# Optimization experiments

Hardware: AMD Instinct MI355X
Metric: run time of the kernel (lower is better)

## Reference

```python
import jax, jax.numpy as jnp
import numpy as np

B, N, F_IN, D, NBLOCKS = 16, 1024, 3, 128, 15
EPS = 1e-5


def setup_inputs() -> dict:
    key = jax.random.key(0)
    ks = jax.random.split(key, 8)
    inputs = jax.random.normal(ks[0], (B, N, F_IN), dtype=jnp.float32)
    # Row-normalized random adjacency as the graph operator L (spectral norm <= 1)
    A = jax.random.uniform(ks[1], (B, N, N), dtype=jnp.float32)
    L = A / jnp.sum(A, axis=-1, keepdims=True)
    mask = (jax.random.uniform(ks[2], (B, N, 1)) < 0.8).astype(jnp.float32)
    mask = mask.at[:, 0, :].set(1.0)  # ensure no empty graph
    W1 = jax.random.normal(ks[3], (F_IN, D), dtype=jnp.float32) / np.sqrt(F_IN)
    b1 = jnp.zeros((D,), jnp.float32)
    W_blocks = jax.random.normal(ks[4], (NBLOCKS, D, D), dtype=jnp.float32) / np.sqrt(D)
    b_blocks = jnp.zeros((NBLOCKS, D), jnp.float32)
    gamma_blocks = jnp.ones((NBLOCKS, D), jnp.float32)
    beta_blocks = jnp.zeros((NBLOCKS, D), jnp.float32)
    gamma1 = jnp.ones((D,), jnp.float32)
    beta1 = jnp.zeros((D,), jnp.float32)
    gamma2 = jnp.ones((D,), jnp.float32)
    beta2 = jnp.zeros((D,), jnp.float32)
    W2 = jax.random.normal(ks[5], (D, D), dtype=jnp.float32) / np.sqrt(D)
    b2 = jnp.zeros((D,), jnp.float32)
    return dict(inputs=inputs, L=L, mask=mask, W1=W1, b1=b1,
                W_blocks=W_blocks, b_blocks=b_blocks,
                gamma_blocks=gamma_blocks, beta_blocks=beta_blocks,
                gamma1=gamma1, beta1=beta1, gamma2=gamma2, beta2=beta2,
                W2=W2, b2=b2)


def _graph_bn(x, gamma, beta):
    # BatchNorm over (batch, nodes) per feature channel (training-mode stats)
    mean = jnp.mean(x, axis=(0, 1), keepdims=True)
    var = jnp.var(x, axis=(0, 1), keepdims=True)
    return (x - mean) * jax.lax.rsqrt(var + EPS) * gamma + beta


def reference(inputs, L, mask, W1, b1, W_blocks, b_blocks,
              gamma_blocks, beta_blocks, gamma1, beta1, gamma2, beta2,
              W2, b2):
    # conv1 (GraphConv k=1): per-node linear
    x1 = jnp.einsum('bnf,fd->bnd', inputs, W1) + b1          # [B,N,D]
    x2 = jnp.zeros_like(x1)

    def step(carry, params):
        a, b_prev = carry
        W, bias, g, be = params
        h = jax.nn.elu(_graph_bn(a, g, be))
        h = jnp.einsum('bnm,bmd->bnd', L, h)                 # Laplacian aggregation
        h = jnp.einsum('bnd,de->bne', h, W) + bias           # LapConv transform
        return (b_prev + h, a), None

    (x1, x2), _ = jax.lax.scan(step, (x1, x2),
                               (W_blocks, b_blocks, gamma_blocks, beta_blocks))

    x = jax.nn.elu(_graph_bn(x1, gamma1, beta1) + _graph_bn(x2, gamma2, beta2))
    # Dropout2d is identity in deterministic/eval reference
    x = jnp.einsum('bnd,de->bne', x, W2) + b2                # conv2 (k=1)
    # masked mean pool over nodes: mask [B,N,1] broadcasts over D
    out = jnp.sum(x * mask, axis=1) / jnp.sum(mask, axis=1)  # [B,D]
    return out
```

## Files before the change

### kernel.cpp

```cpp
#include <hip/hip_runtime.h>

typedef float f32x4 __attribute__((ext_vector_type(4)));
typedef __bf16 bf16x8 __attribute__((ext_vector_type(8)));
typedef unsigned int u32x4 __attribute__((ext_vector_type(4)));
typedef unsigned int u32x2 __attribute__((ext_vector_type(2)));
typedef unsigned short u16;

#define DEV __device__ __forceinline__

DEV u16 f2bf(float f) {
    unsigned int x = __float_as_uint(f);
    x += 0x7fffu + ((x >> 16) & 1u);
    return (u16)(x >> 16);
}
DEV unsigned pk2(float a, float b) {
    return (unsigned)f2bf(a) | ((unsigned)f2bf(b) << 16);
}
DEV float elu(float x) { return x > 0.f ? x : expm1f(x); }

DEV void gload16(const u16* g, void* l) {
    __builtin_amdgcn_global_load_lds(
        (const __attribute__((address_space(1))) unsigned int*)g,
        (__attribute__((address_space(3))) unsigned int*)l,
        16, 0, 0);
}

DEV float aload(const float* p) {
    return __hip_atomic_load(p, __ATOMIC_RELAXED, __HIP_MEMORY_SCOPE_AGENT);
}
DEV void astore(float* p, float v) {
    __hip_atomic_store(p, v, __ATOMIC_RELAXED, __HIP_MEMORY_SCOPE_AGENT);
}

DEV void barw(unsigned* ctr, unsigned cnt) {
    asm volatile("s_waitcnt vmcnt(0) lgkmcnt(0)" ::: "memory");
    __syncthreads();
    if (threadIdx.x == 0) {
        unsigned old = __hip_atomic_fetch_add(ctr, 1u, __ATOMIC_RELAXED,
                                              __HIP_MEMORY_SCOPE_AGENT);
        unsigned tgt = old - (old % cnt) + cnt;
        while (__hip_atomic_load(ctr, __ATOMIC_RELAXED,
                                 __HIP_MEMORY_SCOPE_AGENT) < tgt)
            __builtin_amdgcn_s_sleep(4);
    }
    __syncthreads();
}

constexpr float INV_M = 1.f / 16384.f;
constexpr float EPSV  = 1e-5f;

__global__ __launch_bounds__(256) void k_prep(
        const float* __restrict__ in, const float* __restrict__ L,
        const float* __restrict__ W1, const float* __restrict__ b1,
        const float* __restrict__ Wb,
        u16* __restrict__ Lb, u16* __restrict__ WT,
        float* __restrict__ xA, float* __restrict__ xB,
        float* __restrict__ SP0) {
    int t = threadIdx.x, bid = blockIdx.x;
    {
        long base = (long)bid * 1024;
#pragma unroll
        for (int j = 0; j < 4; ++j) {
            long i = (base + j * 256 + t) * 8;
            f32x4 a = *(const f32x4*)(L + i);
            f32x4 b = *(const f32x4*)(L + i + 4);
            u32x4 v;
            v[0] = pk2(a[0], a[1]); v[1] = pk2(a[2], a[3]);
            v[2] = pk2(b[0], b[1]); v[3] = pk2(b[2], b[3]);
            *(u32x4*)(Lb + i) = v;
        }
    }
    if (bid < 960) {
        int o = bid * 256 + t;
        int kk = o >> 14, r = o & 16383, e = r >> 7, d = r & 127;
        WT[o] = f2bf(Wb[(kk << 14) + (d << 7) + e]);
    }
    if (bid >= 1024 && bid < 1280) {
        __shared__ float red[2][8][128];
        int ib = bid - 1024;
        long R = (long)ib * 64;
        int c4 = (t & 31) * 4, rg = t >> 5;
        float w0[4], w1v[4], w2v[4], bb4[4];
#pragma unroll
        for (int c = 0; c < 4; ++c) {
            w0[c] = W1[c4 + c]; w1v[c] = W1[128 + c4 + c];
            w2v[c] = W1[256 + c4 + c]; bb4[c] = b1[c4 + c];
        }
        float s[4] = {}, q[4] = {};
#pragma unroll
        for (int i = 0; i < 8; ++i) {
            long grow = R + rg + 8 * i;
            float f0 = in[grow * 3], f1 = in[grow * 3 + 1], f2 = in[grow * 3 + 2];
            f32x4 v, z = {0.f, 0.f, 0.f, 0.f};
#pragma unroll
            for (int c = 0; c < 4; ++c) {
                float val = f0 * w0[c] + f1 * w1v[c] + f2 * w2v[c] + bb4[c];
                v[c] = val; s[c] += val; q[c] += val * val;
            }
            *(f32x4*)(xA + grow * 128 + c4) = v;
            *(f32x4*)(xB + grow * 128 + c4) = z;
        }
#pragma unroll
        for (int c = 0; c < 4; ++c) { red[0][rg][c4 + c] = s[c]; red[1][rg][c4 + c] = q[c]; }
        __syncthreads();
        if (t < 128) {
            float a = 0;
#pragma unroll
            for (int g = 0; g < 8; ++g) a += red[0][g][t];
            atomicAdd(&SP0[(ib & 15) * 256 + t], a);
        } else {
            int c = t - 128; float a = 0;
#pragma unroll
            for (int g = 0; g < 8; ++g) a += red[1][g][c];
            atomicAdd(&SP0[(ib & 15) * 256 + 128 + c], a);
        }
    }
}

__global__ __launch_bounds__(512) void k_iter(
        int k,
        const float* __restrict__ mask, const float* __restrict__ bblk,
        const float* __restrict__ gb, const float* __restrict__ beb,
        const float* __restrict__ g1, const float* __restrict__ be1,
        const float* __restrict__ g2, const float* __restrict__ be2,
        const float* __restrict__ W2, const float* __restrict__ b2,
        const u16* __restrict__ Lb, const u16* __restrict__ WT,
        float* __restrict__ xA, float* __restrict__ xB,
        u16* __restrict__ hT, float* __restrict__ SP0, float* __restrict__ SP1,
        unsigned* __restrict__ bar, float* __restrict__ poolP,
        float* __restrict__ maskP, float* __restrict__ out) {
    extern __shared__ char smem[];
    int t = threadIdx.x;
    int bid = blockIdx.x;
    int wg = ((bid & 7) << 5) | (bid >> 3);
    int bb = wg >> 4, n0 = (wg & 15) << 6;
    int l = t & 63, w = t >> 6;
    int wm = w >> 2, wn = w & 3;
    int l16 = l & 15, ld16 = l >> 4;

    float* xcur = (k & 1) ? xB : xA;
    float* spa = (k & 1) ? SP1 : SP0;
    float* spz = (k & 1) ? SP0 : SP1;

    if (k > 0) {
        u16* As = (u16*)smem;
        u16* Bs = (u16*)(smem + 32768);
        float* red = (float*)smem;
        const u16* gA = Lb + ((long)(bb * 1024 + n0)) * 1024;
        const u16* gB = hT + (long)bb * 131072;

        if (k <= 14 && (wg & 15) == 0 && t < 256) astore(&spz[bb * 256 + t], 0.f);

#define STAGE(buf, kt_) do {                                                  \
        int k0_ = (kt_) * 64;                                                 \
        { int u = t; int r = u >> 3, sl = u & 7;                              \
          gload16(gA + (long)r * 1024 + k0_ + ((sl ^ (r & 7)) << 3),          \
                  (char*)As + (buf) * 8192 + u * 16); }                       \
        _Pragma("unroll")                                                     \
        for (int j = 0; j < 2; ++j) {                                         \
            int u = t + 512 * j; int r = u >> 3, sl = u & 7;                  \
            gload16(gB + (long)r * 1024 + k0_ + ((sl ^ (r & 7)) << 3),        \
                    (char*)Bs + (buf) * 16384 + u * 16);                      \
        }                                                                     \
    } while (0)

        f32x4 acc[2][2] = {};
        STAGE(0, 0);
        STAGE(1, 1);
        STAGE(2, 2);
        asm volatile("s_waitcnt vmcnt(6)" ::: "memory");
        __builtin_amdgcn_s_barrier();

        for (int kt = 0; kt < 16; ++kt) {
            if (kt <= 12) STAGE((kt + 3) & 3, kt + 3);
            const char* Ab = (const char*)As + (kt & 3) * 8192;
            const char* Bb = (const char*)Bs + (kt & 3) * 16384;
            __builtin_amdgcn_s_setprio(1);
#pragma unroll
            for (int ks = 0; ks < 2; ++ks) {
                int kb = ks * 64 + ld16 * 16;
                bf16x8 af[2], bfr[2];
#pragma unroll
                for (int m = 0; m < 2; ++m) {
                    int r = wm * 32 + m * 16 + l16;
                    af[m] = *(const bf16x8*)(Ab + r * 128 + (kb ^ ((r & 7) << 4)));
                }
#pragma unroll
                for (int n = 0; n < 2; ++n) {
                    int e = wn * 32 + n * 16 + l16;
                    bfr[n] = *(const bf16x8*)(Bb + e * 128 + (kb ^ ((e & 7) << 4)));
                }
#pragma unroll
                for (int m = 0; m < 2; ++m)
#pragma unroll
                    for (int n = 0; n < 2; ++n)
                        acc[m][n] = __builtin_amdgcn_mfma_f32_16x16x32_bf16(
                            af[m], bfr[n], acc[m][n], 0, 0, 0);
            }
            __builtin_amdgcn_s_setprio(0);
            if (kt <= 12) {
                asm volatile("s_waitcnt vmcnt(6)" ::: "memory");
                __builtin_amdgcn_s_barrier();
            } else if (kt == 13) {
                asm volatile("s_waitcnt vmcnt(3)" ::: "memory");
                __builtin_amdgcn_s_barrier();
            } else if (kt == 14) {
                asm volatile("s_waitcnt vmcnt(0)" ::: "memory");
                __builtin_amdgcn_s_barrier();
            }
        }
#undef STAGE

        float* dst = xcur + (long)wg * 8192;
        const float* biasv = bblk + (k - 1) * 128;
#pragma unroll
        for (int n = 0; n < 2; ++n) {
            int e = wn * 32 + n * 16 + l16;
            float bv = biasv[e];
            float sv = 0.f, qv = 0.f;
#pragma unroll
            for (int m = 0; m < 2; ++m) {
                int row0 = wm * 32 + m * 16 + ld16 * 4;
                float* dp = dst + (long)row0 * 128 + e;
#pragma unroll
                for (int j = 0; j < 4; ++j) {
                    float v = dp[j * 128] + acc[m][n][j] + bv;
                    dp[j * 128] = v;
                    sv += v; qv += v * v;
                }
            }
            red[(wm * 4 + ld16) * 128 + e] = sv;
            red[(8 + wm * 4 + ld16) * 128 + e] = qv;
        }
        __syncthreads();
        if (t < 128) {
            float a = 0;
#pragma unroll
            for (int g = 0; g < 8; ++g) a += red[g * 128 + t];
            atomicAdd(&spa[bb * 256 + t], a);
        } else if (t < 256) {
            int c = t - 128; float a = 0;
#pragma unroll
            for (int g = 0; g < 8; ++g) a += red[(8 + g) * 128 + c];
            atomicAdd(&spa[bb * 256 + 128 + c], a);
        }
        barw(bar, 256);
    }

    if (k < 15) {
        u16* Ws = (u16*)smem;
        u16* Hs = (u16*)(smem + 32768);
        float* st = (float*)(smem + 49152);
        float* sc = (float*)(smem + 50176);
        float* sh = (float*)(smem + 50688);
        if (t < 256) {
            float s = 0.f;
#pragma unroll
            for (int i = 0; i < 16; ++i) s += aload(&spa[i * 256 + t]);
            st[t] = s;
        }
        const u32x4* wsrc = (const u32x4*)(WT + (size_t)k * 16384);
#pragma unroll
        for (int i = 0; i < 4; ++i) {
            int u = t + 512 * i;
            int r = u >> 4, sl = u & 15;
            *(u32x4*)((char*)Ws + r * 256 + ((sl ^ (r & 7)) << 4)) = wsrc[u];
        }
        __syncthreads();
        if (t < 128) {
            float mean = st[t] * INV_M, var = st[128 + t] * INV_M - mean * mean;
            float a = rsqrtf(var + EPSV) * gb[k * 128 + t];
            sc[t] = a; sh[t] = beb[k * 128 + t] - mean * a;
        }
        __syncthreads();
        const float* xb = xcur + (long)wg * 8192;
#pragma unroll
        for (int i = 0; i < 4; ++i) {
            int idx = t + 512 * i;
            int row = idx >> 5, c4 = (idx & 31) * 4;
            f32x4 v = *(const f32x4*)(xb + row * 128 + c4);
            float h0 = elu(v[0] * sc[c4]     + sh[c4]);
            float h1 = elu(v[1] * sc[c4 + 1] + sh[c4 + 1]);
            float h2 = elu(v[2] * sc[c4 + 2] + sh[c4 + 2]);
            float h3 = elu(v[3] * sc[c4 + 3] + sh[c4 + 3]);
            u32x2 pw = {pk2(h0, h1), pk2(h2, h3)};
            *(u32x2*)((char*)Hs + row * 256 + ((c4 * 2) ^ ((row & 7) << 4))) = pw;
        }
        __syncthreads();
        f32x4 acc[2][2] = {};
#pragma unroll
        for (int ks = 0; ks < 4; ++ks) {
            int kb = ks * 64 + ld16 * 16;
            bf16x8 af[2], bfr[2];
#pragma unroll
            for (int m = 0; m < 2; ++m) {
                int r = wm * 32 + m * 16 + l16;
                af[m] = *(const bf16x8*)((char*)Hs + r * 256 + (kb ^ ((r & 7) << 4)));
            }
#pragma unroll
            for (int n = 0; n < 2; ++n) {
                int e = wn * 32 + n * 16 + l16;
                bfr[n] = *(const bf16x8*)((char*)Ws + e * 256 + (kb ^ ((e & 7) << 4)));
            }
#pragma unroll
            for (int m = 0; m < 2; ++m)
#pragma unroll
                for (int n = 0; n < 2; ++n)
                    acc[m][n] = __builtin_amdgcn_mfma_f32_16x16x32_bf16(
                        af[m], bfr[n], acc[m][n], 0, 0, 0);
        }
        __syncthreads();
#pragma unroll
        for (int m = 0; m < 2; ++m)
#pragma unroll
            for (int n = 0; n < 2; ++n) {
                int e = wn * 32 + n * 16 + l16;
                int row0 = wm * 32 + m * 16 + ld16 * 4;
                u32x2 pw = {pk2(acc[m][n][0], acc[m][n][1]),
                            pk2(acc[m][n][2], acc[m][n][3])};
                *(u32x2*)((char*)Hs + e * 128 + ((row0 * 2) ^ ((e & 7) << 4))) = pw;
            }
        __syncthreads();
        {
            int e = t >> 2, sg = t & 3;
            const char* base = (const char*)Hs + e * 128;
            u16* orow = hT + ((long)(bb * 128 + e)) * 1024 + n0 + sg * 16;
#pragma unroll
            for (int u = 0; u < 2; ++u) {
                u32x4 v = *(const u32x4*)(base + ((sg * 32 + u * 16) ^ ((e & 7) << 4)));
                *(u32x4*)(orow + u * 8) = v;
            }
        }
    } else {
        float* x1p = xcur;
        float* x2p = (k & 1) ? xA : xB;
        float* sc1 = (float*)smem;
        float* sh1 = sc1 + 128;
        float* sc2 = sh1 + 128;
        float* sh2 = sc2 + 128;
        float* msk = (float*)(smem + 2048);
        float* fred = (float*)(smem + 4096);
        if (t < 256) {
            int which = t >> 7, c = t & 127;
            const float* p = which ? SP0 : SP1;
            float s = 0.f, q = 0.f;
#pragma unroll
            for (int i = 0; i < 16; ++i) {
                s += aload(&p[i * 256 + c]); q += aload(&p[i * 256 + 128 + c]);
            }
            float mean = s * INV_M, var = q * INV_M - mean * mean;
            float a = rsqrtf(var + EPSV) * (which ? g2[c] : g1[c]);
            (which ? sc2 : sc1)[c] = a;
            (which ? sh2 : sh1)[c] = (which ? be2[c] : be1[c]) - mean * a;
        } else if (t < 320) {
            msk[t - 256] = mask[bb * 1024 + n0 + (t - 256)];
        }
        __syncthreads();
        const float* xb1 = x1p + (long)wg * 8192;
        const float* xb2 = x2p + (long)wg * 8192;
        int row0 = t >> 5, c = (t & 31) * 4;
        f32x4 accv = {0.f, 0.f, 0.f, 0.f};
#pragma unroll
        for (int i = 0; i < 4; ++i) {
            int row = row0 + 16 * i;
            f32x4 v1 = *(const f32x4*)(xb1 + row * 128 + c);
            f32x4 v2 = *(const f32x4*)(xb2 + row * 128 + c);
            float m = msk[row];
            accv[0] += elu(v1[0]*sc1[c]   + sh1[c]   + v2[0]*sc2[c]   + sh2[c])   * m;
            accv[1] += elu(v1[1]*sc1[c+1] + sh1[c+1] + v2[1]*sc2[c+1] + sh2[c+1]) * m;
            accv[2] += elu(v1[2]*sc1[c+2] + sh1[c+2] + v2[2]*sc2[c+2] + sh2[c+2]) * m;
            accv[3] += elu(v1[3]*sc1[c+3] + sh1[c+3] + v2[3]*sc2[c+3] + sh2[c+3]) * m;
        }
        fred[row0 * 128 + c]     = accv[0];
        fred[row0 * 128 + c + 1] = accv[1];
        fred[row0 * 128 + c + 2] = accv[2];
        fred[row0 * 128 + c + 3] = accv[3];
        __syncthreads();
        if (t < 128) {
            float s = 0;
#pragma unroll
            for (int g = 0; g < 16; ++g) s += fred[g * 128 + t];
            astore(&poolP[wg * 128 + t], s);
        }
        if (t == 128) {
            float sm = 0;
#pragma unroll
            for (int j = 0; j < 64; ++j) sm += msk[j];
            astore(&maskP[wg], sm);
        }
        barw(bar, 256);
        if (wg < 16) {
            float* pooled = (float*)smem;
            __syncthreads();
            if (t < 128) {
                float s = 0.f;
                for (int tl = 0; tl < 16; ++tl)
                    s += aload(&poolP[(wg * 16 + tl) * 128 + t]);
                pooled[t] = s;
            }
            if (t == 128) {
                float sm = 0.f;
                for (int tl = 0; tl < 16; ++tl) sm += aload(&maskP[wg * 16 + tl]);
                pooled[128] = 1.f / sm;
            }
            __syncthreads();
            if (t < 128) {
                float acc = 0.f, inv = pooled[128];
                for (int d = 0; d < 128; ++d) acc += pooled[d] * W2[d * 128 + t];
                out[wg * 128 + t] = acc * inv + b2[t];
            }
        }
    }
}


extern "C" void kernel_launch(void* const* d_in, const int* in_sizes, int n_in,
                              void* d_out, int out_size, void* d_ws, size_t ws_size,
                              hipStream_t stream) {
    const float* inputs = (const float*)d_in[0];
    const float* L      = (const float*)d_in[1];
    const float* mask   = (const float*)d_in[2];
    const float* W1     = (const float*)d_in[3];
    const float* b1     = (const float*)d_in[4];
    const float* Wb     = (const float*)d_in[5];
    const float* bblk   = (const float*)d_in[6];
    const float* gb     = (const float*)d_in[7];
    const float* beb    = (const float*)d_in[8];
    const float* g1     = (const float*)d_in[9];
    const float* be1    = (const float*)d_in[10];
    const float* g2     = (const float*)d_in[11];
    const float* be2    = (const float*)d_in[12];
    const float* W2     = (const float*)d_in[13];
    const float* b2     = (const float*)d_in[14];
    float* out = (float*)d_out;

    char* ws = (char*)d_ws;
    u16*      Lb    = (u16*)(ws);
    u16*      WT    = (u16*)(ws + 33554432);
    float*    xA    = (float*)(ws + 34045952);
    float*    xB    = (float*)(ws + 42434560);
    u16*      hT    = (u16*)(ws + 50823168);
    float*    poolP = (float*)(ws + 50823168);
    float*    maskP = (float*)(ws + 50823168 + 131072);
    float*    SP0   = (float*)(ws + 55017472);
    float*    SP1   = (float*)(ws + 55017472 + 16384);
    unsigned* bar   = (unsigned*)(ws + 55017472 + 32768);

    hipMemsetAsync(ws + 55017472, 0, 32768 + 1024, stream);

    hipLaunchKernelGGL(k_prep, dim3(2048), dim3(256), 0, stream,
                       inputs, L, W1, b1, Wb, Lb, WT, xA, xB, SP0);

    for (int k = 0; k <= 15; ++k) {
        hipLaunchKernelGGL(k_iter, dim3(256), dim3(512), 98304, stream, k,
                           mask, bblk, gb, beb, g1, be1, g2, be2, W2, b2,
                           Lb, WT, xA, xB, hT, SP0, SP1, bar, poolP, maskP, out);
    }
}
```

Baseline: 356.2 us.

## Fuse per-block launches into one persistent kernel with per-batch barriers

```diff
diff --git a/kernel.cpp b/kernel.cpp
--- a/kernel.cpp
+++ b/kernel.cpp
@@ -21,8 +21,16 @@
 DEV void gload16(const u16* g, void* l) {
     __builtin_amdgcn_global_load_lds(
         (const __attribute__((address_space(1))) unsigned int*)g,
-        (__attribute__((address_space(3))) unsigned int*)l,
-        16, 0, 0);
+        (__attribute__((address_space(3))) unsigned int*)l, 16, 0, 0);
+}
+DEV void gload16cc(const u16* g, void* l) {
+    __builtin_amdgcn_global_load_lds(
+        (const __attribute__((address_space(1))) unsigned int*)g,
+        (__attribute__((address_space(3))) unsigned int*)l, 16, 0, 17);
+}
+DEV void gstore16cc(u16* p, u32x4 v) {
+    asm volatile("global_store_dwordx4 %0, %1, off sc0 sc1"
+                 :: "v"(p), "v"(v) : "memory");
 }
 
 DEV float aload(const float* p) {
@@ -117,8 +125,7 @@
     }
 }
 
-__global__ __launch_bounds__(512) void k_iter(
-        int k,
+__global__ __launch_bounds__(512) void k_mega(
         const float* __restrict__ mask, const float* __restrict__ bblk,
         const float* __restrict__ gb, const float* __restrict__ beb,
         const float* __restrict__ g1, const float* __restrict__ be1,
@@ -137,58 +144,69 @@
     int l = t & 63, w = t >> 6;
     int wm = w >> 2, wn = w & 3;
     int l16 = l & 15, ld16 = l >> 4;
-
-    float* xcur = (k & 1) ? xB : xA;
-    float* spa = (k & 1) ? SP1 : SP0;
-    float* spz = (k & 1) ? SP0 : SP1;
-
-    if (k > 0) {
-        u16* As = (u16*)smem;
-        u16* Bs = (u16*)(smem + 32768);
-        float* red = (float*)smem;
-        const u16* gA = Lb + ((long)(bb * 1024 + n0)) * 1024;
-        const u16* gB = hT + (long)bb * 131072;
-
-        if (k <= 14 && (wg & 15) == 0 && t < 256) astore(&spz[bb * 256 + t], 0.f);
-
-#define STAGE(buf, kt_) do {                                                  \
-        int k0_ = (kt_) * 64;                                                 \
-        { int u = t; int r = u >> 3, sl = u & 7;                              \
-          gload16(gA + (long)r * 1024 + k0_ + ((sl ^ (r & 7)) << 3),          \
-                  (char*)As + (buf) * 8192 + u * 16); }                       \
-        _Pragma("unroll")                                                     \
-        for (int j = 0; j < 2; ++j) {                                         \
-            int u = t + 512 * j; int r = u >> 3, sl = u & 7;                  \
-            gload16(gB + (long)r * 1024 + k0_ + ((sl ^ (r & 7)) << 3),        \
-                    (char*)Bs + (buf) * 16384 + u * 16);                      \
-        }                                                                     \
-    } while (0)
-
-        f32x4 acc[2][2] = {};
-        STAGE(0, 0);
-        STAGE(1, 1);
-        STAGE(2, 2);
-        asm volatile("s_waitcnt vmcnt(6)" ::: "memory");
-        __builtin_amdgcn_s_barrier();
-
-        for (int kt = 0; kt < 16; ++kt) {
-            if (kt <= 12) STAGE((kt + 3) & 3, kt + 3);
-            const char* Ab = (const char*)As + (kt & 3) * 8192;
-            const char* Bb = (const char*)Bs + (kt & 3) * 16384;
-            __builtin_amdgcn_s_setprio(1);
-#pragma unroll
-            for (int ks = 0; ks < 2; ++ks) {
+    unsigned* barg = bar + 16 + (wg >> 5) * 16;
+
+    for (int k = 0; k < 15; ++k) {
+        float* spa = (k & 1) ? SP1 : SP0;
+        float* spb = (k & 1) ? SP0 : SP1;
+        float* xc  = (k & 1) ? xB : xA;
+        float* xn  = (k & 1) ? xA : xB;
+
+        {
+            u16* Ws = (u16*)smem;
+            u16* Hs = (u16*)(smem + 32768);
+            float* st = (float*)(smem + 49152);
+            float* sc = (float*)(smem + 50176);
+            float* sh = (float*)(smem + 50688);
+            if (t < 256) {
+                float s = 0.f;
+#pragma unroll
+                for (int i = 0; i < 16; ++i) s += aload(&spa[i * 256 + t]);
+                st[t] = s;
+            }
+            if ((wg & 15) == 0 && t < 256) astore(&spb[bb * 256 + t], 0.f);
+            const u32x4* wsrc = (const u32x4*)(WT + (size_t)k * 16384);
+#pragma unroll
+            for (int i = 0; i < 4; ++i) {
+                int u = t + 512 * i;
+                int r = u >> 4, sl = u & 15;
+                *(u32x4*)((char*)Ws + r * 256 + ((sl ^ (r & 7)) << 4)) = wsrc[u];
+            }
+            __syncthreads();
+            if (t < 128) {
+                float mean = st[t] * INV_M, var = st[128 + t] * INV_M - mean * mean;
+                float a = rsqrtf(var + EPSV) * gb[k * 128 + t];
+                sc[t] = a; sh[t] = beb[k * 128 + t] - mean * a;
+            }
+            __syncthreads();
+            const float* xb = xc + (long)wg * 8192;
+#pragma unroll
+            for (int i = 0; i < 4; ++i) {
+                int idx = t + 512 * i;
+                int row = idx >> 5, c4 = (idx & 31) * 4;
+                f32x4 v = *(const f32x4*)(xb + row * 128 + c4);
+                float h0 = elu(v[0] * sc[c4]     + sh[c4]);
+                float h1 = elu(v[1] * sc[c4 + 1] + sh[c4 + 1]);
+                float h2 = elu(v[2] * sc[c4 + 2] + sh[c4 + 2]);
+                float h3 = elu(v[3] * sc[c4 + 3] + sh[c4 + 3]);
+                u32x2 pw = {pk2(h0, h1), pk2(h2, h3)};
+                *(u32x2*)((char*)Hs + row * 256 + ((c4 * 2) ^ ((row & 7) << 4))) = pw;
+            }
+            __syncthreads();
+            f32x4 acc[2][2] = {};
+#pragma unroll
+            for (int ks = 0; ks < 4; ++ks) {
                 int kb = ks * 64 + ld16 * 16;
                 bf16x8 af[2], bfr[2];
 #pragma unroll
                 for (int m = 0; m < 2; ++m) {
                     int r = wm * 32 + m * 16 + l16;
-                    af[m] = *(const bf16x8*)(Ab + r * 128 + (kb ^ ((r & 7) << 4)));
+                    af[m] = *(const bf16x8*)((char*)Hs + r * 256 + (kb ^ ((r & 7) << 4)));
                 }
 #pragma unroll
                 for (int n = 0; n < 2; ++n) {
                     int e = wn * 32 + n * 16 + l16;
-                    bfr[n] = *(const bf16x8*)(Bb + e * 128 + (kb ^ ((e & 7) << 4)));
+                    bfr[n] = *(const bf16x8*)((char*)Ws + e * 256 + (kb ^ ((e & 7) << 4)));
                 }
 #pragma unroll
                 for (int m = 0; m < 2; ++m)
@@ -197,143 +215,138 @@
                         acc[m][n] = __builtin_amdgcn_mfma_f32_16x16x32_bf16(
                             af[m], bfr[n], acc[m][n], 0, 0, 0);
             }
-            __builtin_amdgcn_s_setprio(0);
-            if (kt <= 12) {
-                asm volatile("s_waitcnt vmcnt(6)" ::: "memory");
-                __builtin_amdgcn_s_barrier();
-            } else if (kt == 13) {
-                asm volatile("s_waitcnt vmcnt(3)" ::: "memory");
-                __builtin_amdgcn_s_barrier();
-            } else if (kt == 14) {
-                asm volatile("s_waitcnt vmcnt(0)" ::: "memory");
-                __builtin_amdgcn_s_barrier();
-            }
-        }
+            __syncthreads();
+#pragma unroll
+            for (int m = 0; m < 2; ++m)
+#pragma unroll
+                for (int n = 0; n < 2; ++n) {
+                    int e = wn * 32 + n * 16 + l16;
+                    int row0 = wm * 32 + m * 16 + ld16 * 4;
+                    u32x2 pw = {pk2(acc[m][n][0], acc[m][n][1]),
+                                pk2(acc[m][n][2], acc[m][n][3])};
+                    *(u32x2*)((char*)Hs + e * 128 + ((row0 * 2) ^ ((e & 7) << 4))) = pw;
+                }
+            __syncthreads();
+            {
+                int e = t >> 2, sg = t & 3;
+                const char* base = (const char*)Hs + e * 128;
+                u16* orow = hT + ((long)(bb * 128 + e)) * 1024 + n0 + sg * 16;
+#pragma unroll
+                for (int u = 0; u < 2; ++u) {
+                    u32x4 v = *(const u32x4*)(base + ((sg * 32 + u * 16) ^ ((e & 7) << 4)));
+                    gstore16cc(orow + u * 8, v);
+                }
+            }
+        }
+        barw(barg, 32);
+
+        {
+            u16* As = (u16*)smem;
+            u16* Bs = (u16*)(smem + 32768);
+            float* red = (float*)smem;
+            const u16* gA = Lb + ((long)(bb * 1024 + n0)) * 1024;
+            const u16* gB = hT + (long)bb * 131072;
+
+#define STAGE(buf, kt_) do {                                                  \
+            int k0_ = (kt_) * 64;                                             \
+            { int u = t; int r = u >> 3, sl = u & 7;                          \
+              gload16(gA + (long)r * 1024 + k0_ + ((sl ^ (r & 7)) << 3),      \
+                      (char*)As + (buf) * 8192 + u * 16); }                   \
+            _Pragma("unroll")                                                 \
+            for (int j = 0; j < 2; ++j) {                                     \
+                int u = t + 512 * j; int r = u >> 3, sl = u & 7;              \
+                gload16cc(gB + (long)r * 1024 + k0_ + ((sl ^ (r & 7)) << 3),  \
+                          (char*)Bs + (buf) * 16384 + u * 16);                \
+            }                                                                 \
+        } while (0)
+
+            f32x4 acc[2][2] = {};
+            STAGE(0, 0);
+            STAGE(1, 1);
+            STAGE(2, 2);
+            asm volatile("s_waitcnt vmcnt(6)" ::: "memory");
+            __builtin_amdgcn_s_barrier();
+
+            for (int kt = 0; kt < 16; ++kt) {
+                if (kt <= 12) STAGE((kt + 3) & 3, kt + 3);
+                const char* Ab = (const char*)As + (kt & 3) * 8192;
+                const char* Bb = (const char*)Bs + (kt & 3) * 16384;
+                __builtin_amdgcn_s_setprio(1);
+#pragma unroll
+                for (int ks = 0; ks < 2; ++ks) {
+                    int kb = ks * 64 + ld16 * 16;
+                    bf16x8 af[2], bfr[2];
+#pragma unroll
+                    for (int m = 0; m < 2; ++m) {
+                        int r = wm * 32 + m * 16 + l16;
+                        af[m] = *(const bf16x8*)(Ab + r * 128 + (kb ^ ((r & 7) << 4)));
+                    }
+#pragma unroll
+                    for (int n = 0; n < 2; ++n) {
+                        int e = wn * 32 + n * 16 + l16;
+                        bfr[n] = *(const bf16x8*)(Bb + e * 128 + (kb ^ ((e & 7) << 4)));
+                    }
+#pragma unroll
+                    for (int m = 0; m < 2; ++m)
+#pragma unroll
+                        for (int n = 0; n < 2; ++n)
+                            acc[m][n] = __builtin_amdgcn_mfma_f32_16x16x32_bf16(
+                                af[m], bfr[n], acc[m][n], 0, 0, 0);
+                }
+                __builtin_amdgcn_s_setprio(0);
+                if (kt <= 12) {
+                    asm volatile("s_waitcnt vmcnt(6)" ::: "memory");
+                    __builtin_amdgcn_s_barrier();
+                } else if (kt == 13) {
+                    asm volatile("s_waitcnt vmcnt(3)" ::: "memory");
+                    __builtin_amdgcn_s_barrier();
+                } else if (kt == 14) {
+                    asm volatile("s_waitcnt vmcnt(0)" ::: "memory");
+                    __builtin_amdgcn_s_barrier();
+                }
+            }
 #undef STAGE
 
-        float* dst = xcur + (long)wg * 8192;
-        const float* biasv = bblk + (k - 1) * 128;
-#pragma unroll
-        for (int n = 0; n < 2; ++n) {
-            int e = wn * 32 + n * 16 + l16;
-            float bv = biasv[e];
-            float sv = 0.f, qv = 0.f;
-#pragma unroll
-            for (int m = 0; m < 2; ++m) {
-                int row0 = wm * 32 + m * 16 + ld16 * 4;
-                float* dp = dst + (long)row0 * 128 + e;
-#pragma unroll
-                for (int j = 0; j < 4; ++j) {
-                    float v = dp[j * 128] + acc[m][n][j] + bv;
-                    dp[j * 128] = v;
-                    sv += v; qv += v * v;
-                }
-            }
-            red[(wm * 4 + ld16) * 128 + e] = sv;
-            red[(8 + wm * 4 + ld16) * 128 + e] = qv;
-        }
-        __syncthreads();
-        if (t < 128) {
-            float a = 0;
-#pragma unroll
-            for (int g = 0; g < 8; ++g) a += red[g * 128 + t];
-            atomicAdd(&spa[bb * 256 + t], a);
-        } else if (t < 256) {
-            int c = t - 128; float a = 0;
-#pragma unroll
-            for (int g = 0; g < 8; ++g) a += red[(8 + g) * 128 + c];
-            atomicAdd(&spa[bb * 256 + 128 + c], a);
-        }
-        barw(bar, 256);
-    }
-
-    if (k < 15) {
-        u16* Ws = (u16*)smem;
-        u16* Hs = (u16*)(smem + 32768);
-        float* st = (float*)(smem + 49152);
-        float* sc = (float*)(smem + 50176);
-        float* sh = (float*)(smem + 50688);
-        if (t < 256) {
-            float s = 0.f;
-#pragma unroll
-            for (int i = 0; i < 16; ++i) s += aload(&spa[i * 256 + t]);
-            st[t] = s;
-        }
-        const u32x4* wsrc = (const u32x4*)(WT + (size_t)k * 16384);
-#pragma unroll
-        for (int i = 0; i < 4; ++i) {
-            int u = t + 512 * i;
-            int r = u >> 4, sl = u & 15;
-            *(u32x4*)((char*)Ws + r * 256 + ((sl ^ (r & 7)) << 4)) = wsrc[u];
-        }
-        __syncthreads();
-        if (t < 128) {
-            float mean = st[t] * INV_M, var = st[128 + t] * INV_M - mean * mean;
-            float a = rsqrtf(var + EPSV) * gb[k * 128 + t];
-            sc[t] = a; sh[t] = beb[k * 128 + t] - mean * a;
-        }
-        __syncthreads();
-        const float* xb = xcur + (long)wg * 8192;
-#pragma unroll
-        for (int i = 0; i < 4; ++i) {
-            int idx = t + 512 * i;
-            int row = idx >> 5, c4 = (idx & 31) * 4;
-            f32x4 v = *(const f32x4*)(xb + row * 128 + c4);
-            float h0 = elu(v[0] * sc[c4]     + sh[c4]);
-            float h1 = elu(v[1] * sc[c4 + 1] + sh[c4 + 1]);
-            float h2 = elu(v[2] * sc[c4 + 2] + sh[c4 + 2]);
-            float h3 = elu(v[3] * sc[c4 + 3] + sh[c4 + 3]);
-            u32x2 pw = {pk2(h0, h1), pk2(h2, h3)};
-            *(u32x2*)((char*)Hs + row * 256 + ((c4 * 2) ^ ((row & 7) << 4))) = pw;
-        }
-        __syncthreads();
-        f32x4 acc[2][2] = {};
-#pragma unroll
-        for (int ks = 0; ks < 4; ++ks) {
-            int kb = ks * 64 + ld16 * 16;
-            bf16x8 af[2], bfr[2];
-#pragma unroll
-            for (int m = 0; m < 2; ++m) {
-                int r = wm * 32 + m * 16 + l16;
-                af[m] = *(const bf16x8*)((char*)Hs + r * 256 + (kb ^ ((r & 7) << 4)));
-            }
+            float* dst = xn + (long)wg * 8192;
+            const float* biasv = bblk + k * 128;
 #pragma unroll
             for (int n = 0; n < 2; ++n) {
                 int e = wn * 32 + n * 16 + l16;
-                bfr[n] = *(const bf16x8*)((char*)Ws + e * 256 + (kb ^ ((e & 7) << 4)));
-            }
-#pragma unroll
-            for (int m = 0; m < 2; ++m)
-#pragma unroll
-                for (int n = 0; n < 2; ++n)
-                    acc[m][n] = __builtin_amdgcn_mfma_f32_16x16x32_bf16(
-                        af[m], bfr[n], acc[m][n], 0, 0, 0);
-        }
-        __syncthreads();
-#pragma unroll
-        for (int m = 0; m < 2; ++m)
-#pragma unroll
-            for (int n = 0; n < 2; ++n) {
-                int e = wn * 32 + n * 16 + l16;
-                int row0 = wm * 32 + m * 16 + ld16 * 4;
-                u32x2 pw = {pk2(acc[m][n][0], acc[m][n][1]),
-                            pk2(acc[m][n][2], acc[m][n][3])};
-                *(u32x2*)((char*)Hs + e * 128 + ((row0 * 2) ^ ((e & 7) << 4))) = pw;
-            }
-        __syncthreads();
-        {
-            int e = t >> 2, sg = t & 3;
-            const char* base = (const char*)Hs + e * 128;
-            u16* orow = hT + ((long)(bb * 128 + e)) * 1024 + n0 + sg * 16;
-#pragma unroll
-            for (int u = 0; u < 2; ++u) {
-                u32x4 v = *(const u32x4*)(base + ((sg * 32 + u * 16) ^ ((e & 7) << 4)));
-                *(u32x4*)(orow + u * 8) = v;
-            }
-        }
-    } else {
-        float* x1p = xcur;
-        float* x2p = (k & 1) ? xA : xB;
+                float bv = biasv[e];
+                float sv = 0.f, qv = 0.f;
+#pragma unroll
+                for (int m = 0; m < 2; ++m) {
+                    int row0 = wm * 32 + m * 16 + ld16 * 4;
+                    float* dp = dst + (long)row0 * 128 + e;
+#pragma unroll
+                    for (int j = 0; j < 4; ++j) {
+                        float v = dp[j * 128] + acc[m][n][j] + bv;
+                        dp[j * 128] = v;
+                        sv += v; qv += v * v;
+                    }
+                }
+                red[(wm * 4 + ld16) * 128 + e] = sv;
+                red[(8 + wm * 4 + ld16) * 128 + e] = qv;
+            }
+            __syncthreads();
+            if (t < 128) {
+                float a = 0;
+#pragma unroll
+                for (int g = 0; g < 8; ++g) a += red[g * 128 + t];
+                atomicAdd(&spb[bb * 256 + t], a);
+            } else if (t < 256) {
+                int c = t - 128; float a = 0;
+#pragma unroll
+                for (int g = 0; g < 8; ++g) a += red[(8 + g) * 128 + c];
+                atomicAdd(&spb[bb * 256 + 128 + c], a);
+            }
+        }
+        barw(bar, 256);
+    }
+
+    {
+        float* x1p = xB;
+        float* x2p = xA;
         float* sc1 = (float*)smem;
         float* sh1 = sc1 + 128;
         float* sc2 = sh1 + 128;
@@ -440,20 +453,18 @@
     float*    xA    = (float*)(ws + 34045952);
     float*    xB    = (float*)(ws + 42434560);
     u16*      hT    = (u16*)(ws + 50823168);
-    float*    poolP = (float*)(ws + 50823168);
-    float*    maskP = (float*)(ws + 50823168 + 131072);
+    float*    poolP = (float*)(ws + 55017472 + 40960);
+    float*    maskP = (float*)(ws + 55017472 + 40960 + 131072);
     float*    SP0   = (float*)(ws + 55017472);
     float*    SP1   = (float*)(ws + 55017472 + 16384);
     unsigned* bar   = (unsigned*)(ws + 55017472 + 32768);
 
-    hipMemsetAsync(ws + 55017472, 0, 32768 + 1024, stream);
+    hipMemsetAsync(ws + 55017472, 0, 40960, stream);
 
     hipLaunchKernelGGL(k_prep, dim3(2048), dim3(256), 0, stream,
                        inputs, L, W1, b1, Wb, Lb, WT, xA, xB, SP0);
 
-    for (int k = 0; k <= 15; ++k) {
-        hipLaunchKernelGGL(k_iter, dim3(256), dim3(512), 98304, stream, k,
-                           mask, bblk, gb, beb, g1, be1, g2, be2, W2, b2,
-                           Lb, WT, xA, xB, hT, SP0, SP1, bar, poolP, maskP, out);
-    }
-}
+    hipLaunchKernelGGL(k_mega, dim3(256), dim3(512), 98304, stream,
+                       mask, bblk, gb, beb, g1, be1, g2, be2, W2, b2,
+                       Lb, WT, xA, xB, hT, SP0, SP1, bar, poolP, maskP, out);
+}
```

After: 396.9 us. 1.11x slower.

## Double k_iter workgroup to 1024 threads with one 16-row MFMA tile per wave

Applied to the files above, without the earlier changes.

```diff
diff --git a/kernel.cpp b/kernel.cpp
--- a/kernel.cpp
+++ b/kernel.cpp
@@ -21,8 +21,12 @@
 DEV void gload16(const u16* g, void* l) {
     __builtin_amdgcn_global_load_lds(
         (const __attribute__((address_space(1))) unsigned int*)g,
-        (__attribute__((address_space(3))) unsigned int*)l,
-        16, 0, 0);
+        (__attribute__((address_space(3))) unsigned int*)l, 16, 0, 0);
+}
+DEV void gload4(const u16* g, void* l) {
+    __builtin_amdgcn_global_load_lds(
+        (const __attribute__((address_space(1))) unsigned int*)g,
+        (__attribute__((address_space(3))) unsigned int*)l, 4, 0, 0);
 }
 
 DEV float aload(const float* p) {
@@ -117,7 +121,7 @@
     }
 }
 
-__global__ __launch_bounds__(512) void k_iter(
+__global__ __launch_bounds__(1024) void k_iter(
         int k,
         const float* __restrict__ mask, const float* __restrict__ bblk,
         const float* __restrict__ gb, const float* __restrict__ beb,
@@ -153,18 +157,19 @@
 
 #define STAGE(buf, kt_) do {                                                  \
         int k0_ = (kt_) * 64;                                                 \
-        { int u = t; int r = u >> 3, sl = u & 7;                              \
-          gload16(gA + (long)r * 1024 + k0_ + ((sl ^ (r & 7)) << 3),          \
-                  (char*)As + (buf) * 8192 + u * 16); }                       \
         _Pragma("unroll")                                                     \
         for (int j = 0; j < 2; ++j) {                                         \
-            int u = t + 512 * j; int r = u >> 3, sl = u & 7;                  \
-            gload16(gB + (long)r * 1024 + k0_ + ((sl ^ (r & 7)) << 3),        \
-                    (char*)Bs + (buf) * 16384 + u * 16);                      \
+            int u = t + 1024 * j; int r = u >> 5, s4 = u & 31;                \
+            gload4(gA + (long)r * 1024 + k0_ +                                \
+                       (((s4 >> 2) ^ (r & 7)) << 3) + (s4 & 3) * 2,           \
+                   (char*)As + (buf) * 8192 + u * 4);                         \
         }                                                                     \
+        { int u = t; int r = u >> 3, sl = u & 7;                              \
+          gload16(gB + (long)r * 1024 + k0_ + ((sl ^ (r & 7)) << 3),          \
+                  (char*)Bs + (buf) * 16384 + u * 16); }                      \
     } while (0)
 
-        f32x4 acc[2][2] = {};
+        f32x4 acc[2] = {};
         STAGE(0, 0);
         STAGE(1, 1);
         STAGE(2, 2);
@@ -179,23 +184,18 @@
 #pragma unroll
             for (int ks = 0; ks < 2; ++ks) {
                 int kb = ks * 64 + ld16 * 16;
-                bf16x8 af[2], bfr[2];
-#pragma unroll
-                for (int m = 0; m < 2; ++m) {
-                    int r = wm * 32 + m * 16 + l16;
-                    af[m] = *(const bf16x8*)(Ab + r * 128 + (kb ^ ((r & 7) << 4)));
-                }
+                int r = wm * 16 + l16;
+                bf16x8 af = *(const bf16x8*)(Ab + r * 128 + (kb ^ ((r & 7) << 4)));
+                bf16x8 bfr[2];
 #pragma unroll
                 for (int n = 0; n < 2; ++n) {
                     int e = wn * 32 + n * 16 + l16;
                     bfr[n] = *(const bf16x8*)(Bb + e * 128 + (kb ^ ((e & 7) << 4)));
                 }
 #pragma unroll
-                for (int m = 0; m < 2; ++m)
-#pragma unroll
-                    for (int n = 0; n < 2; ++n)
-                        acc[m][n] = __builtin_amdgcn_mfma_f32_16x16x32_bf16(
-                            af[m], bfr[n], acc[m][n], 0, 0, 0);
+                for (int n = 0; n < 2; ++n)
+                    acc[n] = __builtin_amdgcn_mfma_f32_16x16x32_bf16(
+                        af, bfr[n], acc[n], 0, 0, 0);
             }
             __builtin_amdgcn_s_setprio(0);
             if (kt <= 12) {
@@ -213,35 +213,32 @@
 
         float* dst = xcur + (long)wg * 8192;
         const float* biasv = bblk + (k - 1) * 128;
+        int row0 = wm * 16 + ld16 * 4;
 #pragma unroll
         for (int n = 0; n < 2; ++n) {
             int e = wn * 32 + n * 16 + l16;
             float bv = biasv[e];
             float sv = 0.f, qv = 0.f;
-#pragma unroll
-            for (int m = 0; m < 2; ++m) {
-                int row0 = wm * 32 + m * 16 + ld16 * 4;
-                float* dp = dst + (long)row0 * 128 + e;
-#pragma unroll
-                for (int j = 0; j < 4; ++j) {
-                    float v = dp[j * 128] + acc[m][n][j] + bv;
-                    dp[j * 128] = v;
-                    sv += v; qv += v * v;
-                }
+            float* dp = dst + (long)row0 * 128 + e;
+#pragma unroll
+            for (int j = 0; j < 4; ++j) {
+                float v = dp[j * 128] + acc[n][j] + bv;
+                dp[j * 128] = v;
+                sv += v; qv += v * v;
             }
             red[(wm * 4 + ld16) * 128 + e] = sv;
-            red[(8 + wm * 4 + ld16) * 128 + e] = qv;
+            red[(16 + wm * 4 + ld16) * 128 + e] = qv;
         }
         __syncthreads();
         if (t < 128) {
             float a = 0;
 #pragma unroll
-            for (int g = 0; g < 8; ++g) a += red[g * 128 + t];
+            for (int g = 0; g < 16; ++g) a += red[g * 128 + t];
             atomicAdd(&spa[bb * 256 + t], a);
         } else if (t < 256) {
             int c = t - 128; float a = 0;
 #pragma unroll
-            for (int g = 0; g < 8; ++g) a += red[(8 + g) * 128 + c];
+            for (int g = 0; g < 16; ++g) a += red[(16 + g) * 128 + c];
             atomicAdd(&spa[bb * 256 + 128 + c], a);
         }
         barw(bar, 256);
@@ -261,8 +258,8 @@
         }
         const u32x4* wsrc = (const u32x4*)(WT + (size_t)k * 16384);
 #pragma unroll
-        for (int i = 0; i < 4; ++i) {
-            int u = t + 512 * i;
+        for (int i = 0; i < 2; ++i) {
+            int u = t + 1024 * i;
             int r = u >> 4, sl = u & 15;
             *(u32x4*)((char*)Ws + r * 256 + ((sl ^ (r & 7)) << 4)) = wsrc[u];
         }
@@ -275,8 +272,8 @@
         __syncthreads();
         const float* xb = xcur + (long)wg * 8192;
 #pragma unroll
-        for (int i = 0; i < 4; ++i) {
-            int idx = t + 512 * i;
+        for (int i = 0; i < 2; ++i) {
+            int idx = t + 1024 * i;
             int row = idx >> 5, c4 = (idx & 31) * 4;
             f32x4 v = *(const f32x4*)(xb + row * 128 + c4);
             float h0 = elu(v[0] * sc[c4]     + sh[c4]);
@@ -287,49 +284,39 @@
             *(u32x2*)((char*)Hs + row * 256 + ((c4 * 2) ^ ((row & 7) << 4))) = pw;
         }
         __syncthreads();
-        f32x4 acc[2][2] = {};
+        f32x4 acc2[2] = {};
 #pragma unroll
         for (int ks = 0; ks < 4; ++ks) {
             int kb = ks * 64 + ld16 * 16;
-            bf16x8 af[2], bfr[2];
-#pragma unroll
-            for (int m = 0; m < 2; ++m) {
-                int r = wm * 32 + m * 16 + l16;
-                af[m] = *(const bf16x8*)((char*)Hs + r * 256 + (kb ^ ((r & 7) << 4)));
-            }
+            int r = wm * 16 + l16;
+            bf16x8 af = *(const bf16x8*)((char*)Hs + r * 256 + (kb ^ ((r & 7) << 4)));
+            bf16x8 bfr[2];
 #pragma unroll
             for (int n = 0; n < 2; ++n) {
                 int e = wn * 32 + n * 16 + l16;
                 bfr[n] = *(const bf16x8*)((char*)Ws + e * 256 + (kb ^ ((e & 7) << 4)));
             }
 #pragma unroll
-            for (int m = 0; m < 2; ++m)
-#pragma unroll
-                for (int n = 0; n < 2; ++n)
-                    acc[m][n] = __builtin_amdgcn_mfma_f32_16x16x32_bf16(
-                        af[m], bfr[n], acc[m][n], 0, 0, 0);
-        }
-        __syncthreads();
-#pragma unroll
-        for (int m = 0; m < 2; ++m)
+            for (int n = 0; n < 2; ++n)
+                acc2[n] = __builtin_amdgcn_mfma_f32_16x16x32_bf16(
+                    af, bfr[n], acc2[n], 0, 0, 0);
+        }
+        __syncthreads();
+        {
+            int row0 = wm * 16 + ld16 * 4;
 #pragma unroll
             for (int n = 0; n < 2; ++n) {
                 int e = wn * 32 + n * 16 + l16;
-                int row0 = wm * 32 + m * 16 + ld16 * 4;
-                u32x2 pw = {pk2(acc[m][n][0], acc[m][n][1]),
-                            pk2(acc[m][n][2], acc[m][n][3])};
+                u32x2 pw = {pk2(acc2[n][0], acc2[n][1]),
+                            pk2(acc2[n][2], acc2[n][3])};
                 *(u32x2*)((char*)Hs + e * 128 + ((row0 * 2) ^ ((e & 7) << 4))) = pw;
             }
+        }
         __syncthreads();
         {
-            int e = t >> 2, sg = t & 3;
-            const char* base = (const char*)Hs + e * 128;
-            u16* orow = hT + ((long)(bb * 128 + e)) * 1024 + n0 + sg * 16;
-#pragma unroll
-            for (int u = 0; u < 2; ++u) {
-                u32x4 v = *(const u32x4*)(base + ((sg * 32 + u * 16) ^ ((e & 7) << 4)));
-                *(u32x4*)(orow + u * 8) = v;
-            }
+            int e = t >> 3, sg = t & 7;
+            u32x4 v = *(const u32x4*)((char*)Hs + e * 128 + ((sg * 16) ^ ((e & 7) << 4)));
+            *(u32x4*)(hT + ((long)(bb * 128 + e)) * 1024 + n0 + sg * 8) = v;
         }
     } else {
         float* x1p = xcur;
@@ -361,8 +348,8 @@
         int row0 = t >> 5, c = (t & 31) * 4;
         f32x4 accv = {0.f, 0.f, 0.f, 0.f};
 #pragma unroll
-        for (int i = 0; i < 4; ++i) {
-            int row = row0 + 16 * i;
+        for (int i = 0; i < 2; ++i) {
+            int row = row0 + 32 * i;
             f32x4 v1 = *(const f32x4*)(xb1 + row * 128 + c);
             f32x4 v2 = *(const f32x4*)(xb2 + row * 128 + c);
             float m = msk[row];
@@ -379,7 +366,7 @@
         if (t < 128) {
             float s = 0;
 #pragma unroll
-            for (int g = 0; g < 16; ++g) s += fred[g * 128 + t];
+            for (int g = 0; g < 32; ++g) s += fred[g * 128 + t];
             astore(&poolP[wg * 128 + t], s);
         }
         if (t == 128) {
@@ -452,7 +439,7 @@
                        inputs, L, W1, b1, Wb, Lb, WT, xA, xB, SP0);
 
     for (int k = 0; k <= 15; ++k) {
-        hipLaunchKernelGGL(k_iter, dim3(256), dim3(512), 98304, stream, k,
+        hipLaunchKernelGGL(k_iter, dim3(256), dim3(1024), 98304, stream, k,
                            mask, bblk, gb, beb, g1, be1, g2, be2, W2, b2,
                            Lb, WT, xA, xB, hT, SP0, SP1, bar, poolP, maskP, out);
     }
```

Result: slower. 371.3 us (+4.2%).
